# Performance work log

Hardware: AMD Instinct MI355X
Metric: run time of the kernel (lower is better)

Reference implementation:

```python
import jax, jax.numpy as jnp
import numpy as np

B, N, D = 8, 1024, 256   # batch, nodes, input_size
H, HO = 4, 64            # nhead, hidden_size/nhead
T = 5                    # number of edge types (len(edges))
NEG = -1e9
EPS = 1e-6


def setup_inputs() -> dict:
    key = jax.random.key(0)
    ks = jax.random.split(key, 6)
    nodes_embed = jax.random.normal(ks[0], (B, N, D), dtype=jnp.float32)
    node_adj = jax.random.randint(ks[1], (B, N, N), 0, T + 1)  # values 0..T, 0 = no edge
    # per-head projection W: xavier-ish scale
    W = jax.random.normal(ks[2], (H, D, HO), dtype=jnp.float32) * (1.0 / np.sqrt(D))
    # per-edge-type scoring linear (2*HO -> 1), split into src/dst halves
    a_src = jax.random.normal(ks[3], (H, T, HO), dtype=jnp.float32) * 0.1
    a_dst = jax.random.normal(ks[4], (H, T, HO), dtype=jnp.float32) * 0.1
    bias = jnp.zeros((H, HO), dtype=jnp.float32)
    ln_gamma = jnp.ones((H, HO), dtype=jnp.float32)
    ln_beta = jnp.zeros((H, HO), dtype=jnp.float32)
    return {
        'nodes_embed': nodes_embed,
        'node_adj': node_adj,
        'W': W,
        'a_src': a_src,
        'a_dst': a_dst,
        'bias': bias,
        'ln_gamma': ln_gamma,
        'ln_beta': ln_beta,
    }


def reference(nodes_embed, node_adj, W, a_src, a_dst, bias, ln_gamma, ln_beta):
    # h: [B, H, N, HO] -- all heads projected at once
    h = jnp.einsum('bnd,hde->bhne', nodes_embed, W)
    # The torch code concatenates [h_i, h_j] and applies a (2*HO -> 1) linear per
    # edge type; that equals e_src[t, i] + e_dst[t, j] with the linear weight split
    # into src/dst halves. Avoids materializing the O(N^2 * 2*HO) concat tensor.
    e_src = jnp.einsum('bhne,hte->bhtn', h, a_src)  # [B, H, T, N]
    e_dst = jnp.einsum('bhne,hte->bhtn', h, a_dst)  # [B, H, T, N]
    n_types = a_src.shape[1]
    weight = jnp.zeros(h.shape[:2] + (h.shape[2], h.shape[2]), dtype=h.dtype)  # [B,H,N,N]
    for t in range(n_types):  # small fixed loop over edge types
        mask = (node_adj == t + 1).astype(h.dtype)[:, None]  # [B,1,N,N]
        weight = weight + mask * (e_src[:, :, t, :, None] + e_dst[:, :, t, None, :])
    weight = jax.nn.leaky_relu(weight, negative_slope=0.01)
    weight = jnp.where(node_adj[:, None] == 0, NEG, weight)
    attention = jax.nn.softmax(weight, axis=-1)  # [B,H,N,N]
    dst = jnp.einsum('bhij,bhje->bhie', attention, h) + bias[None, :, None, :]
    out = jax.nn.relu(dst) + h  # dropout is identity (p=0)
    # per-head LayerNorm over HO, eps=1e-6 (biased variance, as torch)
    mu = out.mean(axis=-1, keepdims=True)
    var = out.var(axis=-1, keepdims=True)
    out = (out - mu) / jnp.sqrt(var + EPS) * ln_gamma[None, :, None, :] + ln_beta[None, :, None, :]
    # concat heads: [B,H,N,HO] -> [B,N,H*HO]
    b, hh, n, e = out.shape
    return out.transpose(0, 2, 1, 3).reshape(b, n, hh * e)
```

## Files before the change

kernel.cpp:

```cpp
#include <hip/hip_runtime.h>
#include <hip/hip_bf16.h>

#define Bn 8
#define Nn 1024
#define Dn 256
#define Hn 4
#define HOn 64
#define Tn 5
#define WTR 80

typedef short bf16x8 __attribute__((ext_vector_type(8)));
typedef float f32x4 __attribute__((ext_vector_type(4)));

__device__ __forceinline__ float b2f(unsigned short u) {
    unsigned x = ((unsigned)u) << 16;
    float f;
    __builtin_memcpy(&f, &x, 4);
    return f;
}
__device__ __forceinline__ unsigned bfr(float f) {
    unsigned u;
    __builtin_memcpy(&u, &f, 4);
    return (u + 0x7FFFu + ((u >> 16) & 1u)) >> 16;
}
__device__ __forceinline__ unsigned short f2b(float f) { return (unsigned short)bfr(f); }

__global__ __launch_bounds__(256) void k_signal(float* __restrict__ out, int n) {
    int i = blockIdx.x * 256 + threadIdx.x;
    if (i < n) out[i] = 100.0f;
}

__global__ __launch_bounds__(256) void k_transpose_w(const float* __restrict__ W,
                                                     const float* __restrict__ a_src,
                                                     const float* __restrict__ a_dst,
                                                     unsigned short* __restrict__ WT) {
    __shared__ float tile[64][65];
    int h = blockIdx.x >> 2;
    int d0 = (blockIdx.x & 3) * 64;
    int c0 = threadIdx.x & 63;
    int r0 = threadIdx.x >> 6;
#pragma unroll
    for (int r = 0; r < 16; r++) {
        int d = r * 4 + r0;
        tile[d][c0] = W[((size_t)(h * Dn + d0 + d)) * HOn + c0];
    }
    __syncthreads();
#pragma unroll
    for (int r = 0; r < 16; r++) {
        int e = r * 4 + r0;
        WT[((size_t)(h * WTR + e)) * Dn + d0 + c0] = f2b(tile[c0][e]);
    }
    for (int t = r0; t < 2 * Tn; t += 4) {
        const float* av = (t < Tn) ? (a_src + (h * Tn + t) * HOn)
                                   : (a_dst + (h * Tn + t - Tn) * HOn);
        float s = 0.f;
#pragma unroll
        for (int e = 0; e < HOn; e++) s += tile[c0][e] * av[e];
        WT[((size_t)(h * WTR + 64 + t)) * Dn + d0 + c0] = f2b(s);
    }
    for (int rr = 74 + r0; rr < WTR; rr += 4)
        WT[((size_t)(h * WTR + rr)) * Dn + d0 + c0] = 0;
}

__global__ __launch_bounds__(256) void k_proj(const float* __restrict__ X,
                                              const unsigned short* __restrict__ WT,
                                              const int* __restrict__ adj,
                                              unsigned short* __restrict__ hT,
                                              float* __restrict__ e_src,
                                              float* __restrict__ e_dst,
                                              unsigned* __restrict__ adjp) {
    int tid = threadIdx.x;
    int w = tid >> 6;
    int lane = tid & 63;
    int quad = lane >> 4;
    int l15 = lane & 15;
    int b = blockIdx.x >> 6;
    int i0 = (blockIdx.x & 63) * 16;
    int h = w;
    int bh = b * Hn + h;

    {
        const int* arow = adj + ((size_t)(b * Nn + i0)) * Nn;
        unsigned* aout = adjp + ((size_t)(b * Nn + i0)) * Nn / 4;
#pragma unroll 4
        for (int k = 0; k < 16; k++) {
            int idx = tid + k * 256;
            int4 v = *(const int4*)(arow + (size_t)idx * 4);
            unsigned pk = (unsigned)(v.x & 0xFF) | ((unsigned)(v.y & 0xFF) << 8) |
                          ((unsigned)(v.z & 0xFF) << 16) | ((unsigned)(v.w & 0xFF) << 24);
            aout[idx] = pk;
        }
    }

    bf16x8 Bx[8];
    const float* xf = X + ((size_t)(b * Nn + i0 + l15)) * Dn + quad * 8;
#pragma unroll
    for (int kc = 0; kc < 8; kc++) {
        union { bf16x8 v; unsigned u[4]; } uu;
        const float4* xp = (const float4*)(xf + kc * 32);
        float4 A0 = xp[0], A1 = xp[1];
        __hip_bfloat162 h0 = __float22bfloat162_rn(make_float2(A0.x, A0.y));
        __hip_bfloat162 h1 = __float22bfloat162_rn(make_float2(A0.z, A0.w));
        __hip_bfloat162 h2 = __float22bfloat162_rn(make_float2(A1.x, A1.y));
        __hip_bfloat162 h3 = __float22bfloat162_rn(make_float2(A1.z, A1.w));
        __builtin_memcpy(&uu.u[0], &h0, 4);
        __builtin_memcpy(&uu.u[1], &h1, 4);
        __builtin_memcpy(&uu.u[2], &h2, 4);
        __builtin_memcpy(&uu.u[3], &h3, 4);
        Bx[kc] = uu.v;
    }

    f32x4 acc[5] = {{0.f, 0.f, 0.f, 0.f}, {0.f, 0.f, 0.f, 0.f}, {0.f, 0.f, 0.f, 0.f},
                    {0.f, 0.f, 0.f, 0.f}, {0.f, 0.f, 0.f, 0.f}};
    const unsigned short* wbase = WT + (size_t)h * WTR * Dn;
#pragma unroll
    for (int kc = 0; kc < 8; kc++) {
#pragma unroll
        for (int et = 0; et < 5; et++) {
            bf16x8 Aw = *(const bf16x8*)(wbase + (size_t)(et * 16 + l15) * Dn + kc * 32 + quad * 8);
            acc[et] = __builtin_amdgcn_mfma_f32_16x16x32_bf16(Aw, Bx[kc], acc[et], 0, 0, 0);
        }
    }

#pragma unroll
    for (int et = 0; et < 4; et++) {
#pragma unroll
        for (int reg = 0; reg < 4; reg++) {
            int e = et * 16 + quad * 4 + reg;
            hT[((size_t)bh * HOn + e) * Nn + i0 + l15] = f2b(acc[et][reg]);
        }
    }
#pragma unroll
    for (int reg = 0; reg < 4; reg++) {
        int t = quad * 4 + reg;
        if (t < Tn)
            e_src[((size_t)bh * Tn + t) * Nn + i0 + l15] = acc[4][reg];
        else if (t < 2 * Tn)
            e_dst[((size_t)bh * Tn + (t - Tn)) * Nn + i0 + l15] = acc[4][reg];
    }
}

__global__ __launch_bounds__(512) void k_attn(const unsigned char* __restrict__ adjp,
                                              const float* __restrict__ e_src,
                                              const float* __restrict__ e_dst,
                                              const unsigned short* __restrict__ hT,
                                              const float* __restrict__ bias,
                                              const float* __restrict__ gamma,
                                              const float* __restrict__ beta,
                                              float* __restrict__ out) {
    __shared__ __align__(16) unsigned short p_lds[8][16][136];
    __shared__ float es2[4][16][8];
    __shared__ float l_lds[8][16];
    float* macc = (float*)&p_lds[4][0][0];

    int tid = threadIdx.x;
    int w = tid >> 6;
    int lane = tid & 63;
    int quad = lane >> 4;
    int l15 = lane & 15;
    int hh = w & 3;
    int half = w >> 2;
    int b = blockIdx.x >> 6;
    int i0 = (blockIdx.x & 63) * 16;
    int bh = b * Hn + hh;
    int J0 = half * 512;

    const unsigned char* adj_base = adjp + ((size_t)(b * Nn + i0)) * Nn + J0;
    const float* edst = e_dst + (size_t)bh * Tn * Nn + J0;
    const unsigned short* hTb = hT + (size_t)bh * HOn * Nn;

    f32x4 acc[4] = {{0.f, 0.f, 0.f, 0.f}, {0.f, 0.f, 0.f, 0.f},
                    {0.f, 0.f, 0.f, 0.f}, {0.f, 0.f, 0.f, 0.f}};
    f32x4 accl = {0.f, 0.f, 0.f, 0.f};
    bf16x8 ONES;
    {
        short o = (short)0x3F80;
        ONES = (bf16x8){o, o, o, o, o, o, o, o};
    }

    unsigned bufA[4], bufB[4];
#pragma unroll
    for (int r = 0; r < 4; r++)
        bufA[r] = *(const unsigned short*)(adj_base + (size_t)r * Nn + 2 * lane);
    float2 edc[Tn], edn[Tn];
#pragma unroll
    for (int t = 0; t < Tn; t++) edc[t] = *(const float2*)(edst + t * Nn + 2 * lane);

    if (w < 4) {
        const float* esrc = e_src + (size_t)bh * Tn * Nn;
#pragma unroll
        for (int idx = lane; idx < 80; idx += 64) {
            int t = idx >> 4, row = idx & 15;
            es2[w][row][t] = esrc[t * Nn + i0 + row];
        }
    }
    __syncthreads();

#define P1ROW(ROW, AV)                                                          \
    {                                                                           \
        int a0 = (int)((AV) & 0xFFu);                                           \
        int a1 = (int)(((AV) >> 8) & 0xFFu);                                    \
        int t0 = a0 - 1; t0 = (t0 < 0) ? 0 : t0;                                \
        int t1 = a1 - 1; t1 = (t1 < 0) ? 0 : t1;                                \
        float e0 = es2[hh][ROW][t0];                                            \
        float e1 = es2[hh][ROW][t1];                                            \
        float d0 = edc[0].x, d1 = edc[0].y;                                     \
        d0 = (t0 == 1) ? edc[1].x : d0; d1 = (t1 == 1) ? edc[1].y : d1;         \
        d0 = (t0 == 2) ? edc[2].x : d0; d1 = (t1 == 2) ? edc[2].y : d1;         \
        d0 = (t0 == 3) ? edc[3].x : d0; d1 = (t1 == 3) ? edc[3].y : d1;         \
        d0 = (t0 == 4) ? edc[4].x : d0; d1 = (t1 == 4) ? edc[4].y : d1;         \
        float x0 = e0 + d0; x0 = fmaxf(x0, 0.01f * x0);                         \
        float x1 = e1 + d1; x1 = fmaxf(x1, 0.01f * x1);                         \
        float p0 = __expf(x0); p0 = (a0 == 0) ? 0.f : p0;                       \
        float p1 = __expf(x1); p1 = (a1 == 0) ? 0.f : p1;                       \
        __hip_bfloat162 pp = __float22bfloat162_rn(make_float2(p0, p1));        \
        unsigned pu; __builtin_memcpy(&pu, &pp, 4);                             \
        *(unsigned*)(&p_lds[w][ROW][2 * lane]) = pu;                            \
    }

#pragma unroll 1
    for (int c = 0; c < 4; c++) {
        int jc = c * 128;
#pragma unroll
        for (int r = 0; r < 4; r++)
            bufB[r] = *(const unsigned short*)(adj_base + (size_t)(4 + r) * Nn + jc + 2 * lane);
#pragma unroll
        for (int r = 0; r < 4; r++) P1ROW(r, bufA[r]);
#pragma unroll
        for (int r = 0; r < 4; r++)
            bufA[r] = *(const unsigned short*)(adj_base + (size_t)(8 + r) * Nn + jc + 2 * lane);
        if (c < 3) {
#pragma unroll
            for (int t = 0; t < Tn; t++)
                edn[t] = *(const float2*)(edst + t * Nn + jc + 128 + 2 * lane);
        }
#pragma unroll
        for (int r = 0; r < 4; r++) P1ROW(4 + r, bufB[r]);
#pragma unroll
        for (int r = 0; r < 4; r++)
            bufB[r] = *(const unsigned short*)(adj_base + (size_t)(12 + r) * Nn + jc + 2 * lane);
#pragma unroll
        for (int r = 0; r < 4; r++) P1ROW(8 + r, bufA[r]);
        if (c < 3) {
#pragma unroll
            for (int r = 0; r < 4; r++)
                bufA[r] = *(const unsigned short*)(adj_base + (size_t)r * Nn + jc + 128 + 2 * lane);
        }
#pragma unroll
        for (int r = 0; r < 4; r++) P1ROW(12 + r, bufB[r]);
#pragma unroll
        for (int k = 0; k < 4; k++) {
            bf16x8 Afr = *(const bf16x8*)(&p_lds[w][l15][k * 32 + quad * 8]);
            accl = __builtin_amdgcn_mfma_f32_16x16x32_bf16(Afr, ONES, accl, 0, 0, 0);
#pragma unroll
            for (int et = 0; et < 4; et++) {
                bf16x8 Bf = *(const bf16x8*)(hTb + (size_t)(et * 16 + l15) * Nn + J0 + jc + k * 32 + quad * 8);
                acc[et] = __builtin_amdgcn_mfma_f32_16x16x32_bf16(Afr, Bf, acc[et], 0, 0, 0);
            }
        }
        if (c < 3) {
#pragma unroll
            for (int t = 0; t < Tn; t++) edc[t] = edn[t];
        }
    }
#undef P1ROW

    if (l15 == 0) {
#pragma unroll
        for (int reg = 0; reg < 4; reg++) l_lds[w][quad * 4 + reg] = accl[reg];
    }
    __syncthreads();
    if (w >= 4) {
#pragma unroll
        for (int et = 0; et < 4; et++)
#pragma unroll
            for (int reg = 0; reg < 4; reg++)
                macc[((hh * 16) + quad * 4 + reg) * 64 + et * 16 + l15] = acc[et][reg];
    }
    __syncthreads();
    if (w >= 4) return;

    float bv[4], gv[4], bev[4];
#pragma unroll
    for (int et = 0; et < 4; et++) {
        int e = et * 16 + l15;
        bv[et] = bias[hh * HOn + e];
        gv[et] = gamma[hh * HOn + e];
        bev[et] = beta[hh * HOn + e];
    }
#pragma unroll
    for (int reg = 0; reg < 4; reg++) {
        int r = quad * 4 + reg;
        int i = i0 + r;
        float lw = l_lds[w][r] + l_lds[w + 4][r];
        float linv = 1.f / fmaxf(lw, 1e-30f);
        float dv[4];
        float s = 0.f, ss = 0.f;
#pragma unroll
        for (int et = 0; et < 4; et++) {
            int e = et * 16 + l15;
            float v = (acc[et][reg] + macc[((hh * 16) + r) * 64 + e]) * linv + bv[et];
            v = (v > 0.f) ? v : 0.f;
            v += b2f(hTb[(size_t)e * Nn + i]);
            dv[et] = v;
            s += v;
            ss += v * v;
        }
#pragma unroll
        for (int off = 8; off; off >>= 1) {
            s += __shfl_xor(s, off);
            ss += __shfl_xor(ss, off);
        }
        float mean = s * (1.f / 64.f);
        float var = ss * (1.f / 64.f) - mean * mean;
        float rstd = rsqrtf(var + 1e-6f);
#pragma unroll
        for (int et = 0; et < 4; et++) {
            int e = et * 16 + l15;
            float o = (dv[et] - mean) * rstd * gv[et] + bev[et];
            out[((size_t)(b * Nn + i)) * (Hn * HOn) + hh * HOn + e] = o;
        }
    }
}

extern "C" void kernel_launch(void* const* d_in, const int* in_sizes, int n_in,
                              void* d_out, int out_size, void* d_ws, size_t ws_size,
                              hipStream_t stream) {
    const float* X = (const float*)d_in[0];
    const int* adj = (const int*)d_in[1];
    const float* W = (const float*)d_in[2];
    const float* a_src = (const float*)d_in[3];
    const float* a_dst = (const float*)d_in[4];
    const float* bias = (const float*)d_in[5];
    const float* gamma = (const float*)d_in[6];
    const float* beta = (const float*)d_in[7];
    float* out = (float*)d_out;

    char* ws = (char*)d_ws;
    size_t off = 0;
    unsigned short* hT = (unsigned short*)(ws + off);  off += (size_t)Bn * Hn * Nn * HOn * 2;
    unsigned short* WT = (unsigned short*)(ws + off);  off += (size_t)Hn * WTR * Dn * 2;
    float* e_src = (float*)(ws + off);                 off += (size_t)Bn * Hn * Tn * Nn * 4;
    float* e_dst = (float*)(ws + off);                 off += (size_t)Bn * Hn * Tn * Nn * 4;
    unsigned char* adjp = (unsigned char*)(ws + off);  off += (size_t)Bn * Nn * Nn;

    if (ws_size < off) {
        k_signal<<<(out_size + 255) / 256, 256, 0, stream>>>(out, out_size);
        return;
    }

    k_transpose_w<<<Hn * (Dn / 64), 256, 0, stream>>>(W, a_src, a_dst, WT);
    k_proj<<<Bn * (Nn / 16), 256, 0, stream>>>(X, WT, adj, hT, e_src, e_dst, (unsigned*)adjp);
    k_attn<<<Bn * (Nn / 16), 512, 0, stream>>>(adjp, e_src, e_dst, hT, bias, gamma, beta, out);
}
```

Baseline: 152.8 us.

## Use LDS lookup tables and exp2 with pre-scaled logits in attention

Pre-scales e_src/e_dst by log2(e) in the projection kernel so the attention kernel can call the hardware exp2 directly. The per-element select chain over edge types is replaced by indexed lookups: e_src goes into a 6-entry table with a zero slot for no-edge, and e_dst is staged into a per-wave padded LDS table whose type-0 row holds -3e38, so masked entries give exp2(-huge)=0 without an explicit select. This cuts VALU work in the softmax-numerator loop at the cost of extra LDS traffic and shared memory.

```diff
diff --git a/kernel.cpp b/kernel.cpp
--- a/kernel.cpp
+++ b/kernel.cpp
@@ -8,6 +8,7 @@
 #define HOn 64
 #define Tn 5
 #define WTR 80
+#define EDS 134
 
 typedef short bf16x8 __attribute__((ext_vector_type(8)));
 typedef float f32x4 __attribute__((ext_vector_type(4)));
@@ -24,6 +25,16 @@
     return (u + 0x7FFFu + ((u >> 16) & 1u)) >> 16;
 }
 __device__ __forceinline__ unsigned short f2b(float f) { return (unsigned short)bfr(f); }
+
+__device__ __forceinline__ float fast_exp2(float x) {
+#if __has_builtin(__builtin_amdgcn_exp2f)
+    return __builtin_amdgcn_exp2f(x);
+#else
+    float r;
+    asm("v_exp_f32 %0, %1" : "=v"(r) : "v"(x));
+    return r;
+#endif
+}
 
 __global__ __launch_bounds__(256) void k_signal(float* __restrict__ out, int n) {
     int i = blockIdx.x * 256 + threadIdx.x;
@@ -134,9 +145,9 @@
     for (int reg = 0; reg < 4; reg++) {
         int t = quad * 4 + reg;
         if (t < Tn)
-            e_src[((size_t)bh * Tn + t) * Nn + i0 + l15] = acc[4][reg];
+            e_src[((size_t)bh * Tn + t) * Nn + i0 + l15] = acc[4][reg] * 1.4426950408889634f;
         else if (t < 2 * Tn)
-            e_dst[((size_t)bh * Tn + (t - Tn)) * Nn + i0 + l15] = acc[4][reg];
+            e_dst[((size_t)bh * Tn + (t - Tn)) * Nn + i0 + l15] = acc[4][reg] * 1.4426950408889634f;
     }
 }
 
@@ -151,6 +162,7 @@
     __shared__ __align__(16) unsigned short p_lds[8][16][136];
     __shared__ float es2[4][16][8];
     __shared__ float l_lds[8][16];
+    __shared__ __align__(16) float ed_lds[8][6 * EDS];
     float* macc = (float*)&p_lds[4][0][0];
 
     int tid = threadIdx.x;
@@ -169,6 +181,10 @@
     const float* edst = e_dst + (size_t)bh * Tn * Nn + J0;
     const unsigned short* hTb = hT + (size_t)bh * HOn * Nn;
 
+    int c0 = 2 * lane;
+    int c0w = c0 + (c0 >> 5);
+    float* edw = &ed_lds[w][0];
+
     f32x4 acc[4] = {{0.f, 0.f, 0.f, 0.f}, {0.f, 0.f, 0.f, 0.f},
                     {0.f, 0.f, 0.f, 0.f}, {0.f, 0.f, 0.f, 0.f}};
     f32x4 accl = {0.f, 0.f, 0.f, 0.f};
@@ -178,20 +194,23 @@
         ONES = (bf16x8){o, o, o, o, o, o, o, o};
     }
 
+    edw[c0w] = -3e38f;
+    edw[c0w + 1] = -3e38f;
+
     unsigned bufA[4], bufB[4];
 #pragma unroll
     for (int r = 0; r < 4; r++)
-        bufA[r] = *(const unsigned short*)(adj_base + (size_t)r * Nn + 2 * lane);
-    float2 edc[Tn], edn[Tn];
-#pragma unroll
-    for (int t = 0; t < Tn; t++) edc[t] = *(const float2*)(edst + t * Nn + 2 * lane);
+        bufA[r] = *(const unsigned short*)(adj_base + (size_t)r * Nn + c0);
+    float2 edr[Tn];
+#pragma unroll
+    for (int t = 0; t < Tn; t++) edr[t] = *(const float2*)(edst + t * Nn + c0);
 
     if (w < 4) {
         const float* esrc = e_src + (size_t)bh * Tn * Nn;
 #pragma unroll
-        for (int idx = lane; idx < 80; idx += 64) {
+        for (int idx = lane; idx < 96; idx += 64) {
             int t = idx >> 4, row = idx & 15;
-            es2[w][row][t] = esrc[t * Nn + i0 + row];
+            es2[w][row][t] = t ? esrc[(t - 1) * Nn + i0 + row] : 0.f;
         }
     }
     __syncthreads();
@@ -199,20 +218,15 @@
 #define P1ROW(ROW, AV)                                                          \
     {                                                                           \
         int a0 = (int)((AV) & 0xFFu);                                           \
-        int a1 = (int)(((AV) >> 8) & 0xFFu);                                    \
-        int t0 = a0 - 1; t0 = (t0 < 0) ? 0 : t0;                                \
-        int t1 = a1 - 1; t1 = (t1 < 0) ? 0 : t1;                                \
-        float e0 = es2[hh][ROW][t0];                                            \
-        float e1 = es2[hh][ROW][t1];                                            \
-        float d0 = edc[0].x, d1 = edc[0].y;                                     \
-        d0 = (t0 == 1) ? edc[1].x : d0; d1 = (t1 == 1) ? edc[1].y : d1;         \
-        d0 = (t0 == 2) ? edc[2].x : d0; d1 = (t1 == 2) ? edc[2].y : d1;         \
-        d0 = (t0 == 3) ? edc[3].x : d0; d1 = (t1 == 3) ? edc[3].y : d1;         \
-        d0 = (t0 == 4) ? edc[4].x : d0; d1 = (t1 == 4) ? edc[4].y : d1;         \
+        int a1 = (int)((AV) >> 8);                                              \
+        float e0 = es2[hh][ROW][a0];                                            \
+        float e1 = es2[hh][ROW][a1];                                            \
+        float d0 = edw[a0 * EDS + c0w];                                         \
+        float d1 = edw[a1 * EDS + c0w + 1];                                     \
         float x0 = e0 + d0; x0 = fmaxf(x0, 0.01f * x0);                         \
         float x1 = e1 + d1; x1 = fmaxf(x1, 0.01f * x1);                         \
-        float p0 = __expf(x0); p0 = (a0 == 0) ? 0.f : p0;                       \
-        float p1 = __expf(x1); p1 = (a1 == 0) ? 0.f : p1;                       \
+        float p0 = fast_exp2(x0);                                               \
+        float p1 = fast_exp2(x1);                                               \
         __hip_bfloat162 pp = __float22bfloat162_rn(make_float2(p0, p1));        \
         unsigned pu; __builtin_memcpy(&pu, &pp, 4);                             \
         *(unsigned*)(&p_lds[w][ROW][2 * lane]) = pu;                            \
@@ -222,29 +236,35 @@
     for (int c = 0; c < 4; c++) {
         int jc = c * 128;
 #pragma unroll
+        for (int t = 0; t < Tn; t++) {
+            int wi = (t + 1) * EDS + c0w;
+            edw[wi] = edr[t].x;
+            edw[wi + 1] = edr[t].y;
+        }
+#pragma unroll
         for (int r = 0; r < 4; r++)
-            bufB[r] = *(const unsigned short*)(adj_base + (size_t)(4 + r) * Nn + jc + 2 * lane);
+            bufB[r] = *(const unsigned short*)(adj_base + (size_t)(4 + r) * Nn + jc + c0);
 #pragma unroll
         for (int r = 0; r < 4; r++) P1ROW(r, bufA[r]);
 #pragma unroll
         for (int r = 0; r < 4; r++)
-            bufA[r] = *(const unsigned short*)(adj_base + (size_t)(8 + r) * Nn + jc + 2 * lane);
+            bufA[r] = *(const unsigned short*)(adj_base + (size_t)(8 + r) * Nn + jc + c0);
         if (c < 3) {
 #pragma unroll
             for (int t = 0; t < Tn; t++)
-                edn[t] = *(const float2*)(edst + t * Nn + jc + 128 + 2 * lane);
+                edr[t] = *(const float2*)(edst + t * Nn + jc + 128 + c0);
         }
 #pragma unroll
         for (int r = 0; r < 4; r++) P1ROW(4 + r, bufB[r]);
 #pragma unroll
         for (int r = 0; r < 4; r++)
-            bufB[r] = *(const unsigned short*)(adj_base + (size_t)(12 + r) * Nn + jc + 2 * lane);
+            bufB[r] = *(const unsigned short*)(adj_base + (size_t)(12 + r) * Nn + jc + c0);
 #pragma unroll
         for (int r = 0; r < 4; r++) P1ROW(8 + r, bufA[r]);
         if (c < 3) {
 #pragma unroll
             for (int r = 0; r < 4; r++)
-                bufA[r] = *(const unsigned short*)(adj_base + (size_t)r * Nn + jc + 128 + 2 * lane);
+                bufA[r] = *(const unsigned short*)(adj_base + (size_t)r * Nn + jc + 128 + c0);
         }
 #pragma unroll
         for (int r = 0; r < 4; r++) P1ROW(12 + r, bufB[r]);
@@ -257,10 +277,6 @@
                 bf16x8 Bf = *(const bf16x8*)(hTb + (size_t)(et * 16 + l15) * Nn + J0 + jc + k * 32 + quad * 8);
                 acc[et] = __builtin_amdgcn_mfma_f32_16x16x32_bf16(Afr, Bf, acc[et], 0, 0, 0);
             }
-        }
-        if (c < 3) {
-#pragma unroll
-            for (int t = 0; t < Tn; t++) edc[t] = edn[t];
         }
     }
 #undef P1ROW
```

New measurement: 151.4 us. About the same (-0.9%).
